# Optimization experiments

Hardware: AMD Instinct MI355X
Metric: run time of the kernel (lower is better)

## Reference

```python
import jax, jax.numpy as jnp
import numpy as np
from itertools import product

DIM = 384
HEADS = 8
DIM_HEAD = 64
INNER = HEADS * DIM_HEAD  # 512
KS = 3                    # kernel_size (attention window)
PAD = KS // 2
W_WIN = KS * KS           # 9
SCALE = DIM_HEAD ** -0.5


def setup_inputs() -> dict:
    key = jax.random.key(0)
    k1, k2, k3, k4, k5 = jax.random.split(key, 5)
    B, H, W = 4, 56, 56
    x = jax.random.normal(k1, (B, DIM, H, W), dtype=jnp.float32)
    # 1x1 conv weights stored as (out_ch, in_ch)
    Wq = jax.random.normal(k2, (INNER, DIM), dtype=jnp.float32) * (DIM ** -0.5)
    Wkv = jax.random.normal(k3, (2 * INNER, DIM), dtype=jnp.float32) * (DIM ** -0.5)
    Wo = jax.random.normal(k4, (DIM, INNER), dtype=jnp.float32) * (INNER ** -0.5)
    bo = jax.random.normal(k5, (DIM,), dtype=jnp.float32) * 0.01
    return {"x": x, "Wq": Wq, "Wkv": Wkv, "Wo": Wo, "bo": bo}


def _conv1x1(x, w):
    # x: (B,Cin,H,W), w: (Cout,Cin) -> (B,Cout,H,W)
    return jnp.einsum('bchw,oc->bohw', x, w)


def reference(x, Wq, Wkv, Wo, bo):
    B, C, H, W = x.shape
    q = _conv1x1(x, Wq)                       # (B, INNER, H, W)
    kv = _conv1x1(x, Wkv)                     # (B, 2*INNER, H, W)
    k, v = jnp.split(kv, 2, axis=1)
    # split channels heads-major, matching torch reshape (B, heads, dh, H, W)
    q = q.reshape(B, HEADS, DIM_HEAD, H, W)
    k = k.reshape(B, HEADS, DIM_HEAD, H, W)
    v = v.reshape(B, HEADS, DIM_HEAD, H, W)
    # zero-pad spatial dims (matches F.unfold zero padding: padded taps get logit 0)
    k_pad = jnp.pad(k, ((0, 0), (0, 0), (0, 0), (PAD, PAD), (PAD, PAD)))
    v_pad = jnp.pad(v, ((0, 0), (0, 0), (0, 0), (PAD, PAD), (PAD, PAD)))
    offsets = list(product(range(KS), range(KS)))  # row-major = unfold order
    # dots: (B, heads, H, W, w)
    dots = jnp.stack([
        jnp.einsum('bhdxy,bhdxy->bhxy', q, k_pad[:, :, :, i:i + H, j:j + W])
        for (i, j) in offsets
    ], axis=-1) * SCALE
    attn = jax.nn.softmax(dots, axis=-1)      # softmax over the 9-tap window
    # weighted sum of shifted v: (B, heads, dh, H, W)
    out = sum(
        attn[:, :, None, :, :, w_idx] * v_pad[:, :, :, i:i + H, j:j + W]
        for w_idx, (i, j) in enumerate(offsets)
    )
    out = out.reshape(B, INNER, H, W)
    return _conv1x1(out, Wo) + bo[None, :, None, None]
```

## Files before the change

kernel.cpp:

```cpp
#include <hip/hip_runtime.h>


#define HW 3136
#define WIMG 56
#define QKV_CH 1536
#define SCALE 0.125f
#define SLEN 200

typedef __bf16 bf16x8_t __attribute__((ext_vector_type(8)));
typedef float f32x4_t __attribute__((ext_vector_type(4)));

__device__ __forceinline__ float bf2f(unsigned short u) {
    return __uint_as_float(((unsigned int)u) << 16);
}
__device__ __forceinline__ unsigned short f2bf(float f) {
    unsigned int u = __float_as_uint(f);
    u += 0x7FFFu + ((u >> 16) & 1u);
    return (unsigned short)(u >> 16);
}
__device__ __forceinline__ int gpos(int g, int row) { return (g + ((row >> 1) & 3)) & 3; }

__global__ __launch_bounds__(256) void cvt_w_all(
    const float* __restrict__ Wq, const float* __restrict__ Wkv,
    const float* __restrict__ Wo, unsigned short* __restrict__ wdst)
{
    const int i = blockIdx.x * 256 + threadIdx.x;
    const float* src; int base;
    if (i < 49152)       { src = Wq;  base = 0; }
    else if (i < 147456) { src = Wkv; base = 49152; }
    else                 { src = Wo;  base = 147456; }
    const float4 v = reinterpret_cast<const float4*>(src)[i - base];
    uint2 u;
    u.x = (unsigned int)f2bf(v.x) | ((unsigned int)f2bf(v.y) << 16);
    u.y = (unsigned int)f2bf(v.z) | ((unsigned int)f2bf(v.w) << 16);
    reinterpret_cast<uint2*>(wdst)[i] = u;
}

__global__ __launch_bounds__(256) void cvtT_x(
    const float* __restrict__ x, unsigned short* __restrict__ xT)
{
    __shared__ unsigned short Tl[64 * 36];
    const int sblk = blockIdx.x, kblk = blockIdx.y, b = blockIdx.z;
    const int t = threadIdx.x;

    const float* xp = x + ((size_t)b * 384 + (size_t)kblk * 32) * HW + sblk * 64;
    const int c = t >> 3;
#pragma unroll
    for (int i = 0; i < 2; i++) {
        const int sc = (t & 7) + 8 * i;
        const float4 v = *reinterpret_cast<const float4*>(xp + (size_t)c * HW + sc * 4);
        const int s4 = sc * 4;
        Tl[(s4 + 0) * 36 + c] = f2bf(v.x);
        Tl[(s4 + 1) * 36 + c] = f2bf(v.y);
        Tl[(s4 + 2) * 36 + c] = f2bf(v.z);
        Tl[(s4 + 3) * 36 + c] = f2bf(v.w);
    }
    __syncthreads();

    const int row = t >> 2, gran = t & 3;
    const uint2 lo = *reinterpret_cast<const uint2*>(&Tl[row * 36 + gran * 8]);
    const uint2 hi = *reinterpret_cast<const uint2*>(&Tl[row * 36 + gran * 8 + 4]);
    uint4 o; o.x = lo.x; o.y = lo.y; o.z = hi.x; o.w = hi.y;
    unsigned short* dst = xT + ((((size_t)b * 49 + sblk) * 12 + kblk) << 11);
    *reinterpret_cast<uint4*>(dst + t * 8) = o;
}

__global__ __launch_bounds__(256) void gemm1(
    const unsigned short* __restrict__ xT,
    const unsigned short* __restrict__ Wb,
    unsigned short* __restrict__ qkv)
{
    __shared__ __align__(16) unsigned short A_lds[128 * 32];
    __shared__ __align__(16) unsigned short B_lds[64 * 32];

    const int sblk = blockIdx.x;
    const int o0 = blockIdx.y * 128;
    const int b  = blockIdx.z;
    const int t  = threadIdx.x;
    const int lane = t & 63, w = t >> 6;
    const int quad = lane >> 4, mrow = lane & 15;

    const int ar = t >> 2, ag = t & 3;
    const unsigned short* wr0 = Wb + (size_t)(o0 + ar) * 384;
    const unsigned short* wr1 = Wb + (size_t)(o0 + 64 + ar) * 384;
    const unsigned short* xsrc = xT + (((size_t)b * 49 + sblk) * 12 << 11)
                               + w * 512 + lane * 8;

    f32x4_t acc[2][4];
#pragma unroll
    for (int m = 0; m < 2; m++)
#pragma unroll
        for (int nt = 0; nt < 4; nt++) acc[m][nt] = (f32x4_t){0.f, 0.f, 0.f, 0.f};

    for (int kb = 0; kb < 12; kb++) {
        const uint4 a0 = *reinterpret_cast<const uint4*>(wr0 + kb * 32 + ag * 8);
        const uint4 a1 = *reinterpret_cast<const uint4*>(wr1 + kb * 32 + ag * 8);

        __syncthreads();
        __builtin_amdgcn_global_load_lds(
            (const __attribute__((address_space(1))) unsigned int*)(xsrc + (size_t)kb * 2048),
            (__attribute__((address_space(3))) unsigned int*)(B_lds + w * 512),
            16, 0, 0);
        *reinterpret_cast<uint4*>(&A_lds[ar * 32 + gpos(ag, ar) * 8]) = a0;
        *reinterpret_cast<uint4*>(&A_lds[(64 + ar) * 32 + gpos(ag, 64 + ar) * 8]) = a1;
        __syncthreads();

        bf16x8_t bfr[4];
#pragma unroll
        for (int nt = 0; nt < 4; nt++)
            bfr[nt] = *reinterpret_cast<const bf16x8_t*>(&B_lds[(nt * 16 + mrow) * 32 + quad * 8]);
#pragma unroll
        for (int m = 0; m < 2; m++) {
            const int orow = w * 32 + m * 16 + mrow;
            const bf16x8_t af = *reinterpret_cast<const bf16x8_t*>(&A_lds[orow * 32 + gpos(quad, orow) * 8]);
#pragma unroll
            for (int nt = 0; nt < 4; nt++)
                acc[m][nt] = __builtin_amdgcn_mfma_f32_16x16x32_bf16(af, bfr[nt], acc[m][nt], 0, 0, 0);
        }
    }

    const int s0 = sblk * 64;
#pragma unroll
    for (int m = 0; m < 2; m++)
#pragma unroll
        for (int nt = 0; nt < 4; nt++)
#pragma unroll
            for (int r = 0; r < 4; r++) {
                const int oo = o0 + w * 32 + m * 16 + quad * 4 + r;
                const int ss = s0 + nt * 16 + mrow;
                qkv[(size_t)b * QKV_CH * HW + (size_t)oo * HW + ss] = f2bf(acc[m][nt][r]);
            }
}

__global__ __launch_bounds__(256) void gemm3(
    const unsigned short* __restrict__ ao,
    const unsigned short* __restrict__ Wb,
    const float* __restrict__ bias,
    float* __restrict__ out)
{
    __shared__ __align__(16) unsigned short A_lds[128 * 32];
    __shared__ __align__(16) unsigned short B_lds[64 * 32];

    const int s0 = blockIdx.x * 64;
    const int o0 = blockIdx.y * 128;
    const int b  = blockIdx.z;
    const int t  = threadIdx.x;
    const int lane = t & 63, w = t >> 6;
    const int quad = lane >> 4, mrow = lane & 15;

    const int ar = t >> 2, ag = t & 3;
    const int bs = t & 63, bg = t >> 6;

    const unsigned short* xp = ao + (size_t)b * 512 * HW + s0 + bs;
    const unsigned short* wr0 = Wb + (size_t)(o0 + ar) * 512;
    const unsigned short* wr1 = Wb + (size_t)(o0 + 64 + ar) * 512;

    f32x4_t acc[2][4];
#pragma unroll
    for (int m = 0; m < 2; m++)
#pragma unroll
        for (int nt = 0; nt < 4; nt++) acc[m][nt] = (f32x4_t){0.f, 0.f, 0.f, 0.f};

    for (int k0 = 0; k0 < 512; k0 += 32) {
        const uint4 a0 = *reinterpret_cast<const uint4*>(wr0 + k0 + ag * 8);
        const uint4 a1 = *reinterpret_cast<const uint4*>(wr1 + k0 + ag * 8);
        __align__(16) unsigned short bv[8];
#pragma unroll
        for (int j = 0; j < 8; j++)
            bv[j] = xp[(size_t)(k0 + bg * 8 + j) * HW];

        __syncthreads();
        *reinterpret_cast<uint4*>(&A_lds[ar * 32 + gpos(ag, ar) * 8]) = a0;
        *reinterpret_cast<uint4*>(&A_lds[(64 + ar) * 32 + gpos(ag, 64 + ar) * 8]) = a1;
        *reinterpret_cast<uint4*>(&B_lds[bs * 32 + gpos(bg, bs) * 8]) =
            *reinterpret_cast<const uint4*>(bv);
        __syncthreads();

        bf16x8_t bfr[4];
#pragma unroll
        for (int nt = 0; nt < 4; nt++) {
            const int srow = nt * 16 + mrow;
            bfr[nt] = *reinterpret_cast<const bf16x8_t*>(&B_lds[srow * 32 + gpos(quad, srow) * 8]);
        }
#pragma unroll
        for (int m = 0; m < 2; m++) {
            const int orow = w * 32 + m * 16 + mrow;
            const bf16x8_t af = *reinterpret_cast<const bf16x8_t*>(&A_lds[orow * 32 + gpos(quad, orow) * 8]);
#pragma unroll
            for (int nt = 0; nt < 4; nt++)
                acc[m][nt] = __builtin_amdgcn_mfma_f32_16x16x32_bf16(af, bfr[nt], acc[m][nt], 0, 0, 0);
        }
    }

#pragma unroll
    for (int m = 0; m < 2; m++)
#pragma unroll
        for (int nt = 0; nt < 4; nt++)
#pragma unroll
            for (int r = 0; r < 4; r++) {
                const int oo = o0 + w * 32 + m * 16 + quad * 4 + r;
                const int ss = s0 + nt * 16 + mrow;
                out[(size_t)b * 384 * HW + (size_t)oo * HW + ss] = acc[m][nt][r] + bias[oo];
            }
}

__global__ __launch_bounds__(256) void natt2(
    const unsigned short* __restrict__ qkv,
    unsigned short* __restrict__ ao)
{
    __shared__ __align__(16) unsigned short smem[2 * 64 * SLEN];
    unsigned short* Kl = smem;
    unsigned short* Vl = smem + 64 * SLEN;
    float* dred = reinterpret_cast<float*>(smem);

    const int t = threadIdx.x, lane = t & 63, w = t >> 6;
    const int s0 = blockIdx.x * 64;
    const int s  = s0 + lane;
    const int h  = blockIdx.y, b = blockIdx.z;
    const int y  = s / WIMG, xx = s % WIMG;

    const size_t hbase = (size_t)b * QKV_CH * HW + (size_t)(h * 64) * HW;
    const unsigned short* kg = qkv + hbase + (size_t)512 * HW;
    const unsigned short* vg = qkv + hbase + (size_t)1024 * HW;

#pragma unroll
    for (int i = 0; i < 6; i++) {
        const int f = i * 256 + t;
        const int d = f / 24, j = f % 24;
        int g = s0 - 64 + j * 8;
        g = min(max(g, 0), HW - 8);
        const uint4 k4 = *reinterpret_cast<const uint4*>(kg + (size_t)d * HW + g);
        const uint4 v4 = *reinterpret_cast<const uint4*>(vg + (size_t)d * HW + g);
        *reinterpret_cast<uint4*>(&Kl[d * SLEN + j * 8]) = k4;
        *reinterpret_cast<uint4*>(&Vl[d * SLEN + j * 8]) = v4;
    }

    int   off9[9];
    float msk[9];
#pragma unroll
    for (int ty = 0; ty < 3; ty++)
#pragma unroll
        for (int tx = 0; tx < 3; tx++) {
            const int tap = ty * 3 + tx;
            const int ny = y + ty - 1, nx = xx + tx - 1;
            const bool v = (ny >= 0) && (ny < WIMG) && (nx >= 0) && (nx < WIMG);
            off9[tap] = v ? ((ty - 1) * WIMG + (tx - 1)) : 0;
            msk[tap]  = v ? 1.f : 0.f;
        }

    __syncthreads();

    const unsigned short* qp = qkv + hbase + s;
    float dots[9];
#pragma unroll
    for (int tp = 0; tp < 9; tp++) dots[tp] = 0.f;
#pragma unroll 4
    for (int dd = 0; dd < 16; dd++) {
        const int d = w * 16 + dd;
        const float qv = bf2f(qp[(size_t)d * HW]);
        const int bi = d * SLEN + lane + 64;
#pragma unroll
        for (int tp = 0; tp < 9; tp++)
            dots[tp] += qv * bf2f(Kl[bi + off9[tp]]);
    }

    __syncthreads();
#pragma unroll
    for (int tp = 0; tp < 9; tp++) dred[(tp * 4 + w) * 64 + lane] = dots[tp];
    __syncthreads();

    float mx = -1e30f, dt[9];
#pragma unroll
    for (int tp = 0; tp < 9; tp++) {
        const float sum = dred[(tp * 4 + 0) * 64 + lane] + dred[(tp * 4 + 1) * 64 + lane] +
                          dred[(tp * 4 + 2) * 64 + lane] + dred[(tp * 4 + 3) * 64 + lane];
        dt[tp] = msk[tp] * (sum * SCALE);
        mx = fmaxf(mx, dt[tp]);
    }
    float se = 0.f, w9[9];
#pragma unroll
    for (int tp = 0; tp < 9; tp++) { w9[tp] = __expf(dt[tp] - mx); se += w9[tp]; }
    const float inv = 1.f / se;
#pragma unroll
    for (int tp = 0; tp < 9; tp++) w9[tp] *= inv * msk[tp];

    unsigned short* aop = ao + (size_t)b * 512 * HW + (size_t)(h * 64) * HW + s;
#pragma unroll 4
    for (int dd = 0; dd < 16; dd++) {
        const int d = w * 16 + dd;
        const int bi = d * SLEN + lane + 64;
        float o = 0.f;
#pragma unroll
        for (int tp = 0; tp < 9; tp++)
            o += w9[tp] * bf2f(Vl[bi + off9[tp]]);
        aop[(size_t)d * HW] = f2bf(o);
    }
}

extern "C" void kernel_launch(void* const* d_in, const int* in_sizes, int n_in,
                              void* d_out, int out_size, void* d_ws, size_t ws_size,
                              hipStream_t stream) {
    const float* x   = (const float*)d_in[0];
    const float* Wq  = (const float*)d_in[1];
    const float* Wkv = (const float*)d_in[2];
    const float* Wo  = (const float*)d_in[3];
    const float* bo  = (const float*)d_in[4];
    float* out = (float*)d_out;

    unsigned short* xT   = (unsigned short*)d_ws;
    unsigned short* wb   = xT + (size_t)4 * 384 * HW;
    unsigned short* wob  = wb + (size_t)1536 * 384;
    unsigned short* qkvb = wob + (size_t)384 * 512;
    unsigned short* aob  = qkvb + (size_t)4 * QKV_CH * HW;

    cvt_w_all<<<dim3(768), 256, 0, stream>>>(Wq, Wkv, Wo, wb);
    cvtT_x<<<dim3(49, 12, 4), 256, 0, stream>>>(x, xT);

    gemm1<<<dim3(49, 12, 4), 256, 0, stream>>>(xT, wb, qkvb);
    natt2<<<dim3(49, 8, 4), 256, 0, stream>>>(qkvb, aob);
    gemm3<<<dim3(49, 3, 4), 256, 0, stream>>>(aob, wob, bo, out);
}
```

Before: 152.1 us.

## Enlarge gemm1 tile to 128x128 with pre-tiled weight and activation layouts

After: 149.5 us. Within noise of the previous version (-1.7%).

```diff
diff --git a/kernel.cpp b/kernel.cpp
--- a/kernel.cpp
+++ b/kernel.cpp
@@ -20,20 +20,41 @@
 }
 __device__ __forceinline__ int gpos(int g, int row) { return (g + ((row >> 1) & 3)) & 3; }
 
-__global__ __launch_bounds__(256) void cvt_w_all(
+__global__ __launch_bounds__(256) void cvt_w(
     const float* __restrict__ Wq, const float* __restrict__ Wkv,
-    const float* __restrict__ Wo, unsigned short* __restrict__ wdst)
+    const float* __restrict__ Wo,
+    unsigned short* __restrict__ wT, unsigned short* __restrict__ wob)
 {
     const int i = blockIdx.x * 256 + threadIdx.x;
-    const float* src; int base;
-    if (i < 49152)       { src = Wq;  base = 0; }
-    else if (i < 147456) { src = Wkv; base = 49152; }
-    else                 { src = Wo;  base = 147456; }
-    const float4 v = reinterpret_cast<const float4*>(src)[i - base];
-    uint2 u;
-    u.x = (unsigned int)f2bf(v.x) | ((unsigned int)f2bf(v.y) << 16);
-    u.y = (unsigned int)f2bf(v.z) | ((unsigned int)f2bf(v.w) << 16);
-    reinterpret_cast<uint2*>(wdst)[i] = u;
+    if (i < 73728) {
+        const int g = i & 3;
+        const int idx3 = i >> 2;
+        const int o128 = idx3 & 127;
+        const int rest = idx3 >> 7;
+        const int kb = rest % 12, oblk = rest / 12;
+        const int o = oblk * 128 + o128;
+        const int k0 = kb * 32 + g * 8;
+        const float* src = (o < 512) ? (Wq + (size_t)o * 384 + k0)
+                                     : (Wkv + (size_t)(o - 512) * 384 + k0);
+        const float4 v0 = *reinterpret_cast<const float4*>(src);
+        const float4 v1 = *reinterpret_cast<const float4*>(src + 4);
+        uint4 u;
+        u.x = (unsigned int)f2bf(v0.x) | ((unsigned int)f2bf(v0.y) << 16);
+        u.y = (unsigned int)f2bf(v0.z) | ((unsigned int)f2bf(v0.w) << 16);
+        u.z = (unsigned int)f2bf(v1.x) | ((unsigned int)f2bf(v1.y) << 16);
+        u.w = (unsigned int)f2bf(v1.z) | ((unsigned int)f2bf(v1.w) << 16);
+        reinterpret_cast<uint4*>(wT)[i] = u;
+    } else {
+        const int j = i - 73728;
+        const float4 v0 = reinterpret_cast<const float4*>(Wo)[j * 2];
+        const float4 v1 = reinterpret_cast<const float4*>(Wo)[j * 2 + 1];
+        uint4 u;
+        u.x = (unsigned int)f2bf(v0.x) | ((unsigned int)f2bf(v0.y) << 16);
+        u.y = (unsigned int)f2bf(v0.z) | ((unsigned int)f2bf(v0.w) << 16);
+        u.z = (unsigned int)f2bf(v1.x) | ((unsigned int)f2bf(v1.y) << 16);
+        u.w = (unsigned int)f2bf(v1.z) | ((unsigned int)f2bf(v1.w) << 16);
+        reinterpret_cast<uint4*>(wob)[j] = u;
+    }
 }
 
 __global__ __launch_bounds__(256) void cvtT_x(
@@ -42,6 +63,12 @@
     __shared__ unsigned short Tl[64 * 36];
     const int sblk = blockIdx.x, kblk = blockIdx.y, b = blockIdx.z;
     const int t = threadIdx.x;
+
+    if (sblk == 49) {
+        unsigned short* dst = xT + (((size_t)b * 25 + 24) * 12 + kblk) * 4096 + 2048;
+        *reinterpret_cast<uint4*>(dst + t * 8) = (uint4){0, 0, 0, 0};
+        return;
+    }
 
     const float* xp = x + ((size_t)b * 384 + (size_t)kblk * 32) * HW + sblk * 64;
     const int c = t >> 3;
@@ -61,75 +88,79 @@
     const uint2 lo = *reinterpret_cast<const uint2*>(&Tl[row * 36 + gran * 8]);
     const uint2 hi = *reinterpret_cast<const uint2*>(&Tl[row * 36 + gran * 8 + 4]);
     uint4 o; o.x = lo.x; o.y = lo.y; o.z = hi.x; o.w = hi.y;
-    unsigned short* dst = xT + ((((size_t)b * 49 + sblk) * 12 + kblk) << 11);
+    unsigned short* dst = xT + (((size_t)b * 25 + (sblk >> 1)) * 12 + kblk) * 4096
+                        + (sblk & 1) * 2048;
     *reinterpret_cast<uint4*>(dst + t * 8) = o;
 }
 
 __global__ __launch_bounds__(256) void gemm1(
     const unsigned short* __restrict__ xT,
-    const unsigned short* __restrict__ Wb,
+    const unsigned short* __restrict__ wT,
     unsigned short* __restrict__ qkv)
 {
     __shared__ __align__(16) unsigned short A_lds[128 * 32];
-    __shared__ __align__(16) unsigned short B_lds[64 * 32];
+    __shared__ __align__(16) unsigned short B_lds[128 * 32];
 
     const int sblk = blockIdx.x;
-    const int o0 = blockIdx.y * 128;
+    const int oblk = blockIdx.y;
     const int b  = blockIdx.z;
     const int t  = threadIdx.x;
     const int lane = t & 63, w = t >> 6;
     const int quad = lane >> 4, mrow = lane & 15;
-
-    const int ar = t >> 2, ag = t & 3;
-    const unsigned short* wr0 = Wb + (size_t)(o0 + ar) * 384;
-    const unsigned short* wr1 = Wb + (size_t)(o0 + 64 + ar) * 384;
-    const unsigned short* xsrc = xT + (((size_t)b * 49 + sblk) * 12 << 11)
-                               + w * 512 + lane * 8;
-
-    f32x4_t acc[2][4];
-#pragma unroll
-    for (int m = 0; m < 2; m++)
-#pragma unroll
-        for (int nt = 0; nt < 4; nt++) acc[m][nt] = (f32x4_t){0.f, 0.f, 0.f, 0.f};
+    const int wm = w >> 1, wn = w & 1;
+
+    const unsigned short* wsrc = wT + ((size_t)oblk * 12) * 4096;
+    const unsigned short* xsrc = xT + (((size_t)b * 25 + sblk) * 12) * 4096;
+
+    f32x4_t acc[4][4];
+#pragma unroll
+    for (int m = 0; m < 4; m++)
+#pragma unroll
+        for (int n = 0; n < 4; n++) acc[m][n] = (f32x4_t){0.f, 0.f, 0.f, 0.f};
 
     for (int kb = 0; kb < 12; kb++) {
-        const uint4 a0 = *reinterpret_cast<const uint4*>(wr0 + kb * 32 + ag * 8);
-        const uint4 a1 = *reinterpret_cast<const uint4*>(wr1 + kb * 32 + ag * 8);
+        const uint4 a0 = *reinterpret_cast<const uint4*>(wsrc + (size_t)kb * 4096 + t * 8);
+        const uint4 a1 = *reinterpret_cast<const uint4*>(wsrc + (size_t)kb * 4096 + 2048 + t * 8);
+        const uint4 b0 = *reinterpret_cast<const uint4*>(xsrc + (size_t)kb * 4096 + t * 8);
+        const uint4 b1 = *reinterpret_cast<const uint4*>(xsrc + (size_t)kb * 4096 + 2048 + t * 8);
 
         __syncthreads();
-        __builtin_amdgcn_global_load_lds(
-            (const __attribute__((address_space(1))) unsigned int*)(xsrc + (size_t)kb * 2048),
-            (__attribute__((address_space(3))) unsigned int*)(B_lds + w * 512),
-            16, 0, 0);
-        *reinterpret_cast<uint4*>(&A_lds[ar * 32 + gpos(ag, ar) * 8]) = a0;
-        *reinterpret_cast<uint4*>(&A_lds[(64 + ar) * 32 + gpos(ag, 64 + ar) * 8]) = a1;
+        *reinterpret_cast<uint4*>(A_lds + t * 8) = a0;
+        *reinterpret_cast<uint4*>(A_lds + 2048 + t * 8) = a1;
+        *reinterpret_cast<uint4*>(B_lds + t * 8) = b0;
+        *reinterpret_cast<uint4*>(B_lds + 2048 + t * 8) = b1;
         __syncthreads();
 
-        bf16x8_t bfr[4];
-#pragma unroll
-        for (int nt = 0; nt < 4; nt++)
-            bfr[nt] = *reinterpret_cast<const bf16x8_t*>(&B_lds[(nt * 16 + mrow) * 32 + quad * 8]);
-#pragma unroll
-        for (int m = 0; m < 2; m++) {
-            const int orow = w * 32 + m * 16 + mrow;
-            const bf16x8_t af = *reinterpret_cast<const bf16x8_t*>(&A_lds[orow * 32 + gpos(quad, orow) * 8]);
-#pragma unroll
-            for (int nt = 0; nt < 4; nt++)
-                acc[m][nt] = __builtin_amdgcn_mfma_f32_16x16x32_bf16(af, bfr[nt], acc[m][nt], 0, 0, 0);
+        bf16x8_t af[4], bf[4];
+#pragma unroll
+        for (int m = 0; m < 4; m++)
+            af[m] = *reinterpret_cast<const bf16x8_t*>(&A_lds[(wm * 64 + m * 16 + mrow) * 32 + quad * 8]);
+#pragma unroll
+        for (int n = 0; n < 4; n++)
+            bf[n] = *reinterpret_cast<const bf16x8_t*>(&B_lds[(wn * 64 + n * 16 + mrow) * 32 + quad * 8]);
+#pragma unroll
+        for (int m = 0; m < 4; m++)
+#pragma unroll
+            for (int n = 0; n < 4; n++)
+                acc[m][n] = __builtin_amdgcn_mfma_f32_16x16x32_bf16(af[m], bf[n], acc[m][n], 0, 0, 0);
+    }
+
+    const int o0 = oblk * 128 + wm * 64;
+    const int s0 = sblk * 128 + wn * 64;
+    unsigned short* outb = qkv + (size_t)b * QKV_CH * HW;
+#pragma unroll
+    for (int m = 0; m < 4; m++)
+#pragma unroll
+        for (int n = 0; n < 4; n++) {
+            const int ss = s0 + n * 16 + mrow;
+            if (ss < HW) {
+#pragma unroll
+                for (int r = 0; r < 4; r++) {
+                    const int oo = o0 + m * 16 + quad * 4 + r;
+                    outb[(size_t)oo * HW + ss] = f2bf(acc[m][n][r]);
+                }
+            }
         }
-    }
-
-    const int s0 = sblk * 64;
-#pragma unroll
-    for (int m = 0; m < 2; m++)
-#pragma unroll
-        for (int nt = 0; nt < 4; nt++)
-#pragma unroll
-            for (int r = 0; r < 4; r++) {
-                const int oo = o0 + w * 32 + m * 16 + quad * 4 + r;
-                const int ss = s0 + nt * 16 + mrow;
-                qkv[(size_t)b * QKV_CH * HW + (size_t)oo * HW + ss] = f2bf(acc[m][nt][r]);
-            }
 }
 
 __global__ __launch_bounds__(256) void gemm3(
@@ -308,15 +339,15 @@
     float* out = (float*)d_out;
 
     unsigned short* xT   = (unsigned short*)d_ws;
-    unsigned short* wb   = xT + (size_t)4 * 384 * HW;
-    unsigned short* wob  = wb + (size_t)1536 * 384;
-    unsigned short* qkvb = wob + (size_t)384 * 512;
+    unsigned short* wT   = xT + (size_t)4915200;
+    unsigned short* wob  = wT + (size_t)589824;
+    unsigned short* qkvb = wob + (size_t)196608;
     unsigned short* aob  = qkvb + (size_t)4 * QKV_CH * HW;
 
-    cvt_w_all<<<dim3(768), 256, 0, stream>>>(Wq, Wkv, Wo, wb);
-    cvtT_x<<<dim3(49, 12, 4), 256, 0, stream>>>(x, xT);
-
-    gemm1<<<dim3(49, 12, 4), 256, 0, stream>>>(xT, wb, qkvb);
+    cvt_w<<<dim3(384), 256, 0, stream>>>(Wq, Wkv, Wo, wT, wob);
+    cvtT_x<<<dim3(50, 12, 4), 256, 0, stream>>>(x, xT);
+
+    gemm1<<<dim3(25, 12, 4), 256, 0, stream>>>(xT, wT, qkvb);
     natt2<<<dim3(49, 8, 4), 256, 0, stream>>>(qkvb, aob);
     gemm3<<<dim3(49, 3, 4), 256, 0, stream>>>(aob, wob, bo, out);
 }
```
